# Kernel tuning notes

Measured on AMD Instinct MI355X. Metric: run time of the kernel, lower is better.

Reference implementation:

```python
import jax, jax.numpy as jnp
import numpy as np

# Segmented linear polynomial: irreps '96x0e + 64x1o + 32x2e' -> same
MULS_IN = (96, 64, 32)   # input multiplicities per irrep segment
MULS_OUT = (96, 64, 32)  # output multiplicities per irrep segment
IRREP_DIMS = (1, 3, 5)   # 2l+1 for l = 0, 1, 2
NUM_ELEMENTS = 64        # number of indexed weight sets
BATCH = 16384            # nodes
IN_SIZE = sum(m * d for m, d in zip(MULS_IN, IRREP_DIMS))    # 448
OUT_SIZE = sum(m * d for m, d in zip(MULS_OUT, IRREP_DIMS))  # 448
W_SIZE = sum(mi * mo for mi, mo in zip(MULS_IN, MULS_OUT))   # 14336


def setup_inputs() -> dict:
    key = jax.random.key(0)
    k1, k2, k3 = jax.random.split(key, 3)
    weights = jax.random.normal(k1, (NUM_ELEMENTS, W_SIZE), dtype=jnp.float32)
    x = jax.random.normal(k2, (BATCH, IN_SIZE), dtype=jnp.float32)
    weight_indices = jax.random.randint(k3, (BATCH,), 0, NUM_ELEMENTS, dtype=jnp.int64)
    return {"weights": weights, "x": x, "weight_indices": weight_indices}


def reference(weights, x, weight_indices):
    """Indexed segmented linear: per irrep segment,
    y[b, o, m] = sum_i x[b, i, m] * W[idx[b], i, o]."""
    B = x.shape[0]
    outs = []
    w_off = 0
    x_off = 0
    for mi, mo, d in zip(MULS_IN, MULS_OUT, IRREP_DIMS):
        W_seg = weights[:, w_off:w_off + mi * mo].reshape(-1, mi, mo)  # [E, mi, mo]
        x_seg = x[:, x_off:x_off + mi * d].reshape(B, mi, d)           # [B, mi, d]
        Wg = W_seg[weight_indices]                                     # [B, mi, mo] gather
        y_seg = jnp.einsum('bim,bio->bom', x_seg, Wg)                  # [B, mo, d]
        outs.append(y_seg.reshape(B, mo * d))
        w_off += mi * mo
        x_off += mi * d
    return jnp.concatenate(outs, axis=1)  # [B, OUT_SIZE]
```

## Files before the change

kernel.cpp:

```cpp
#include <hip/hip_runtime.h>


#define BATCH     16384
#define IN_SIZE   448
#define OUT_SIZE  448
#define W_SIZE    14336
#define NELEM     64
#define RTILE     32
#define MAXTILES  576
#define WT_ELEM   15872

typedef __attribute__((ext_vector_type(8))) short short8;
typedef __attribute__((ext_vector_type(8))) unsigned short us8;
typedef __attribute__((ext_vector_type(4))) float f32x4;

__device__ __forceinline__ unsigned short f2bf(float f) {
    unsigned int u = __float_as_uint(f);
    u += 0x7fffu + ((u >> 16) & 1u);
    return (unsigned short)(u >> 16);
}


template <int MI, int MO, int SRC, int DB>
__device__ __forceinline__ void wprep_seg(const float* __restrict__ we,
                                          unsigned short* __restrict__ de,
                                          unsigned short* lw, int t) {
    constexpr int LP  = MO + 4;
    constexpr int STR = MI + 8;
    constexpr int CNT = MI * MO;
    constexpr int C8  = STR / 8;

    for (int g = t * 4; g < CNT; g += 1024) {
        const int i = g / MO, o = g - i * MO;
        const float4 v = *(const float4*)(we + SRC + g);
        ushort4 w = { f2bf(v.x), f2bf(v.y), f2bf(v.z), f2bf(v.w) };
        *(ushort4*)&lw[i * LP + o] = w;
    }
    __syncthreads();

    for (int c = t; c < MO * C8; c += 256) {
        const int o = c / C8, i0 = (c - o * C8) * 8;
        us8 w;
        #pragma unroll
        for (int k = 0; k < 8; ++k)
            w[k] = (i0 + k < MI) ? lw[(i0 + k) * LP + o] : (unsigned short)0;
        *(us8*)&de[DB + o * STR + i0] = w;
    }
}

__global__ __launch_bounds__(256) void combo_kernel(
    const int* __restrict__ widx, const float* __restrict__ weights,
    int* __restrict__ hists, unsigned short* __restrict__ wt) {
    __shared__ __align__(16) unsigned short lw[9600];
    __shared__ int h[NELEM];
    const int t = threadIdx.x;

    if (blockIdx.x < 192) {
        const int e = blockIdx.x / 3, seg = blockIdx.x - 3 * (blockIdx.x / 3);
        const float* __restrict__ we = weights + (size_t)e * W_SIZE;
        unsigned short* __restrict__ de = wt + (size_t)e * WT_ELEM;
        if (seg == 0)      wprep_seg<96, 96,     0,     0>(we, de, lw, t);
        else if (seg == 1) wprep_seg<64, 64,  9216,  9984>(we, de, lw, t);
        else               wprep_seg<32, 32, 13312, 14592>(we, de, lw, t);
        return;
    }
    const int b = blockIdx.x - 192;
    if (t < NELEM) h[t] = 0;
    __syncthreads();
    atomicAdd(&h[widx[b * 256 + t]], 1);
    __syncthreads();
    if (t < NELEM) hists[b * NELEM + t] = h[t];
}


__global__ __launch_bounds__(256) void scatter_kernel(
    const int* __restrict__ widx, const int* __restrict__ hists,
    int* __restrict__ offsets, int* __restrict__ tileoff, int* __restrict__ blk2e,
    int* __restrict__ rowids) {
    __shared__ int tot_s[NELEM], pre_s[NELEM], base_s[NELEM];
    __shared__ int off_s[NELEM + 1], tl_s[NELEM + 1];
    const int b = blockIdx.x, t = threadIdx.x;

    if (t < NELEM) {
        int before = 0, tot = 0;
        for (int c = 0; c < 64; ++c) {
            const int h = hists[c * NELEM + t];
            before += (c < b) ? h : 0;
            tot += h;
        }
        tot_s[t] = tot; pre_s[t] = before;
    }
    __syncthreads();
    if (t == 0) {
        int o = 0, tl = 0;
        for (int e = 0; e < NELEM; ++e) {
            off_s[e] = o; tl_s[e] = tl;
            o += tot_s[e]; tl += (tot_s[e] + RTILE - 1) >> 5;
        }
        off_s[NELEM] = o; tl_s[NELEM] = tl;
    }
    __syncthreads();
    if (t < NELEM) base_s[t] = off_s[t] + pre_s[t];

    if (b == 0) {
        if (t < NELEM) { offsets[t] = off_s[t]; tileoff[t] = tl_s[t]; }
        if (t == 0)    { offsets[NELEM] = off_s[NELEM]; tileoff[NELEM] = tl_s[NELEM]; }
        for (int i = t; i < MAXTILES; i += 256) blk2e[i] = -1;
        __syncthreads();
        if (t < NELEM)
            for (int bb = tl_s[t]; bb < tl_s[t + 1]; ++bb) blk2e[bb] = t;
    }
    __syncthreads();

    const int row = b * 256 + t;
    const int e = widx[row];
    const int pos = atomicAdd(&base_s[e], 1);
    rowids[pos] = row;
}


template <int MI, int MO, int D, int XOFF, int YOFF, int WB>
__device__ __forceinline__ void do_seg(const float* __restrict__ x,
                                       const unsigned short* __restrict__ wt_e,
                                       const int* rid_s, int nrows,
                                       float* __restrict__ out,
                                       unsigned short* lds_w, unsigned short* lds_x,
                                       int t) {
    constexpr int XP   = MI * D + 8;
    constexpr int WSTR = MI + 8;
    constexpr int NT   = MO / 16;
    constexpr int KB   = MI / 32;
    constexpr int MTL  = 2 * D;
    constexpr int WCH  = (MO * WSTR) / 8;
    constexpr int FPT  = (MI * D) / 8;
    constexpr int NQ   = FPT / 4;
    constexpr int MOD  = MO * D;
    constexpr int NTW  = (MTL * NT) / 4;
    constexpr int F4R  = MOD / 4;

    const int r = t >> 3, j = t & 7;

    const float4* __restrict__ src =
        (const float4*)(x + (size_t)rid_s[r] * IN_SIZE + XOFF + j * FPT);
    float vv[FPT];
    #pragma unroll
    for (int q = 0; q < NQ; ++q) {
        const float4 v = src[q];
        vv[q * 4 + 0] = v.x; vv[q * 4 + 1] = v.y;
        vv[q * 4 + 2] = v.z; vv[q * 4 + 3] = v.w;
    }

    const uint4* __restrict__ wsrc = (const uint4*)(wt_e + WB);
    for (int idx = t; idx < WCH; idx += 256) ((uint4*)lds_w)[idx] = wsrc[idx];

    if (D == 1) {
        #pragma unroll
        for (int q = 0; q < NQ; ++q) {
            ushort4 w = { f2bf(vv[q * 4 + 0]), f2bf(vv[q * 4 + 1]),
                          f2bf(vv[q * 4 + 2]), f2bf(vv[q * 4 + 3]) };
            *(ushort4*)&lds_x[r * XP + j * FPT + q * 4] = w;
        }
    } else if (D == 3) {
        #pragma unroll
        for (int m = 0; m < 3; ++m) {
            us8 w;
            #pragma unroll
            for (int bq = 0; bq < 8; ++bq) w[bq] = f2bf(vv[3 * bq + m]);
            *(us8*)&lds_x[r * XP + m * MI + j * 8] = w;
        }
    } else {
        #pragma unroll
        for (int m = 0; m < 5; ++m) {
            ushort4 w = { f2bf(vv[m]), f2bf(vv[5 + m]),
                          f2bf(vv[10 + m]), f2bf(vv[15 + m]) };
            *(ushort4*)&lds_x[r * XP + m * MI + j * 4] = w;
        }
    }
    __syncthreads();

    const int lane = t & 63, w = t >> 6;
    const int row_l = lane & 15, kg = lane >> 4;
    f32x4 accs[NTW];
    #pragma unroll
    for (int q = 0; q < NTW; ++q) {
        const int ct = w + q * 4;
        const int mIdx = ct / NT, nt = ct - mIdx * NT;
        const int mt = mIdx & 1, mch = mIdx >> 1;
        f32x4 acc = {0.f, 0.f, 0.f, 0.f};
        #pragma unroll
        for (int kb = 0; kb < KB; ++kb) {
            const short8 a = *(const short8*)&lds_x[(mt * 16 + row_l) * XP + mch * MI + kb * 32 + kg * 8];
            const short8 b = *(const short8*)&lds_w[(nt * 16 + row_l) * WSTR + kb * 32 + kg * 8];
            acc = __builtin_amdgcn_mfma_f32_16x16x32_bf16(a, b, acc, 0, 0, 0);
        }
        accs[q] = acc;
    }
    __syncthreads();

    float* __restrict__ lout = (float*)lds_w;
    #pragma unroll
    for (int q = 0; q < NTW; ++q) {
        const int ct = w + q * 4;
        const int mIdx = ct / NT, nt = ct - mIdx * NT;
        const int mt = mIdx & 1, mch = mIdx >> 1;
        const int o = nt * 16 + row_l;
        #pragma unroll
        for (int jj = 0; jj < 4; ++jj) {
            const int m = mt * 16 + kg * 4 + jj;
            lout[m * MOD + o * D + mch] = accs[q][jj];
        }
    }
    __syncthreads();

    for (int idx = t; idx < RTILE * F4R; idx += 256) {
        const int rr = idx / F4R, c = idx - rr * F4R;
        if (rr < nrows) {
            float4 v = *(const float4*)&lout[rr * MOD + c * 4];
            *(float4*)&out[(size_t)rid_s[rr] * OUT_SIZE + YOFF + c * 4] = v;
        }
    }
    __syncthreads();
}

__global__ __launch_bounds__(256) void gemm_kernel(
    const float* __restrict__ x, const unsigned short* __restrict__ wt,
    const int* __restrict__ rowids, const int* __restrict__ offsets,
    const int* __restrict__ tileoff, const int* __restrict__ blk2e,
    float* __restrict__ out) {
    __shared__ __align__(16) unsigned short lds[13312];
    __shared__ int rid_s[RTILE];

    const int t   = threadIdx.x;
    const int seg = blockIdx.x / MAXTILES;
    const int tb  = blockIdx.x - seg * MAXTILES;
    const int e   = blk2e[tb];
    if (e < 0) return;
    const int tile  = tb - tileoff[e];
    const int r0    = offsets[e];
    const int cnt   = offsets[e + 1] - r0;
    const int rbase = r0 + tile * RTILE;
    const int nrows = min(RTILE, cnt - tile * RTILE);
    if (t < RTILE) rid_s[t] = rowids[rbase + min(t, nrows - 1)];
    __syncthreads();

    const unsigned short* wt_e = wt + (size_t)e * WT_ELEM;
    if (seg == 0)
        do_seg<96, 96, 1,   0,   0,     0>(x, wt_e, rid_s, nrows, out, lds, lds + 9984, t);
    else if (seg == 1)
        do_seg<64, 64, 3,  96,  96,  9984>(x, wt_e, rid_s, nrows, out, lds, lds + 4608, t);
    else
        do_seg<32, 32, 5, 288, 288, 14592>(x, wt_e, rid_s, nrows, out, lds, lds + 1280, t);
}


extern "C" void kernel_launch(void* const* d_in, const int* in_sizes, int n_in,
                              void* d_out, int out_size, void* d_ws, size_t ws_size,
                              hipStream_t stream) {
    const float* weights = (const float*)d_in[0];
    const float* x       = (const float*)d_in[1];
    const int*   widx    = (const int*)d_in[2];
    float*       out     = (float*)d_out;

    char* ws = (char*)d_ws;
    int* hists   = (int*)(ws + 0);
    int* offsets = (int*)(ws + 16384);
    int* tileoff = (int*)(ws + 16896);
    int* blk2e   = (int*)(ws + 17408);
    int* rowids  = (int*)(ws + 20480);
    unsigned short* wt = (unsigned short*)(ws + 86016);

    combo_kernel  <<<256, 256, 0, stream>>>(widx, weights, hists, wt);
    scatter_kernel<<<64,  256, 0, stream>>>(widx, hists, offsets, tileoff, blk2e, rowids);
    gemm_kernel   <<<3 * MAXTILES, 256, 0, stream>>>(x, wt, rowids, offsets, tileoff, blk2e, out);
}
```

Before: 32.04 us.

## Drop scatter kernel; derive tile row ids in-GEMM via ballot prefix scan

Removes the separate scatter kernel. A single block in the combo kernel now builds the full histogram, offsets and tile map, and each GEMM block rebuilds its own 32 row ids by scanning all weight indices with per-thread bitmasks, a wave prefix sum and popcount. This saves one kernel launch and the rowids buffer round-trip. In exchange every GEMM block reads the whole 64KB index array, and the histogram is done serially by one block. A trailing barrier in the segment routine is also dropped.

```diff
diff --git a/kernel.cpp b/kernel.cpp
--- a/kernel.cpp
+++ b/kernel.cpp
@@ -50,9 +50,9 @@
 
 __global__ __launch_bounds__(256) void combo_kernel(
     const int* __restrict__ widx, const float* __restrict__ weights,
-    int* __restrict__ hists, unsigned short* __restrict__ wt) {
+    int* __restrict__ offsets, int* __restrict__ tileoff, int* __restrict__ blk2e,
+    unsigned short* __restrict__ wt) {
     __shared__ __align__(16) unsigned short lw[9600];
-    __shared__ int h[NELEM];
     const int t = threadIdx.x;
 
     if (blockIdx.x < 192) {
@@ -64,58 +64,28 @@
         else               wprep_seg<32, 32, 13312, 14592>(we, de, lw, t);
         return;
     }
-    const int b = blockIdx.x - 192;
+
+    __shared__ int h[NELEM];
+    __shared__ int off_s[NELEM + 1], tl_s[NELEM + 1];
     if (t < NELEM) h[t] = 0;
     __syncthreads();
-    atomicAdd(&h[widx[b * 256 + t]], 1);
-    __syncthreads();
-    if (t < NELEM) hists[b * NELEM + t] = h[t];
-}
-
-
-__global__ __launch_bounds__(256) void scatter_kernel(
-    const int* __restrict__ widx, const int* __restrict__ hists,
-    int* __restrict__ offsets, int* __restrict__ tileoff, int* __restrict__ blk2e,
-    int* __restrict__ rowids) {
-    __shared__ int tot_s[NELEM], pre_s[NELEM], base_s[NELEM];
-    __shared__ int off_s[NELEM + 1], tl_s[NELEM + 1];
-    const int b = blockIdx.x, t = threadIdx.x;
-
-    if (t < NELEM) {
-        int before = 0, tot = 0;
-        for (int c = 0; c < 64; ++c) {
-            const int h = hists[c * NELEM + t];
-            before += (c < b) ? h : 0;
-            tot += h;
-        }
-        tot_s[t] = tot; pre_s[t] = before;
-    }
+    for (int i = 0; i < 64; ++i)
+        atomicAdd(&h[widx[i * 256 + t]], 1);
     __syncthreads();
     if (t == 0) {
         int o = 0, tl = 0;
         for (int e = 0; e < NELEM; ++e) {
             off_s[e] = o; tl_s[e] = tl;
-            o += tot_s[e]; tl += (tot_s[e] + RTILE - 1) >> 5;
+            o += h[e]; tl += (h[e] + RTILE - 1) >> 5;
         }
         off_s[NELEM] = o; tl_s[NELEM] = tl;
     }
     __syncthreads();
-    if (t < NELEM) base_s[t] = off_s[t] + pre_s[t];
-
-    if (b == 0) {
-        if (t < NELEM) { offsets[t] = off_s[t]; tileoff[t] = tl_s[t]; }
-        if (t == 0)    { offsets[NELEM] = off_s[NELEM]; tileoff[NELEM] = tl_s[NELEM]; }
-        for (int i = t; i < MAXTILES; i += 256) blk2e[i] = -1;
-        __syncthreads();
-        if (t < NELEM)
-            for (int bb = tl_s[t]; bb < tl_s[t + 1]; ++bb) blk2e[bb] = t;
-    }
-    __syncthreads();
-
-    const int row = b * 256 + t;
-    const int e = widx[row];
-    const int pos = atomicAdd(&base_s[e], 1);
-    rowids[pos] = row;
+    if (t <= NELEM) { offsets[t] = off_s[t]; tileoff[t] = tl_s[t]; }
+    for (int i = t; i < MAXTILES; i += 256) blk2e[i] = -1;
+    __syncthreads();
+    if (t < NELEM)
+        for (int bb = tl_s[t]; bb < tl_s[t + 1]; ++bb) blk2e[bb] = t;
 }
 
 
@@ -219,16 +189,16 @@
             *(float4*)&out[(size_t)rid_s[rr] * OUT_SIZE + YOFF + c * 4] = v;
         }
     }
-    __syncthreads();
 }
 
 __global__ __launch_bounds__(256) void gemm_kernel(
     const float* __restrict__ x, const unsigned short* __restrict__ wt,
-    const int* __restrict__ rowids, const int* __restrict__ offsets,
+    const int* __restrict__ widx, const int* __restrict__ offsets,
     const int* __restrict__ tileoff, const int* __restrict__ blk2e,
     float* __restrict__ out) {
     __shared__ __align__(16) unsigned short lds[13312];
     __shared__ int rid_s[RTILE];
+    __shared__ int wsum[4];
 
     const int t   = threadIdx.x;
     const int seg = blockIdx.x / MAXTILES;
@@ -236,12 +206,43 @@
     const int e   = blk2e[tb];
     if (e < 0) return;
     const int tile  = tb - tileoff[e];
-    const int r0    = offsets[e];
-    const int cnt   = offsets[e + 1] - r0;
-    const int rbase = r0 + tile * RTILE;
-    const int nrows = min(RTILE, cnt - tile * RTILE);
-    if (t < RTILE) rid_s[t] = rowids[rbase + min(t, nrows - 1)];
-    __syncthreads();
+    const int cnt   = offsets[e + 1] - offsets[e];
+    const int lo    = tile * RTILE;
+    const int nrows = min(RTILE, cnt - lo);
+
+    {
+        unsigned long long m = 0;
+        #pragma unroll
+        for (int i = 0; i < 64; ++i)
+            m |= (unsigned long long)(widx[i * 256 + t] == e) << i;
+        const int c = __popcll(m);
+        int xacc = c;
+        #pragma unroll
+        for (int d = 1; d < 64; d <<= 1) {
+            const int v = __shfl_up(xacc, d, 64);
+            if ((t & 63) >= d) xacc += v;
+        }
+        if ((t & 63) == 63) wsum[t >> 6] = xacc;
+        __syncthreads();
+        int wbase = 0;
+        #pragma unroll
+        for (int wv = 0; wv < 4; ++wv) wbase += (wv < (t >> 6)) ? wsum[wv] : 0;
+        const int p = wbase + xacc - c;
+        if (p < lo + RTILE && p + c > lo) {
+            unsigned long long mm = m;
+            int k = p;
+            while (mm) {
+                const int i = __ffsll((long long)mm) - 1;
+                if (k >= lo) rid_s[k - lo] = i * 256 + t;
+                ++k;
+                if (k >= lo + RTILE) break;
+                mm &= mm - 1;
+            }
+        }
+        __syncthreads();
+        if (t >= nrows && t < RTILE) rid_s[t] = rid_s[0];
+        __syncthreads();
+    }
 
     const unsigned short* wt_e = wt + (size_t)e * WT_ELEM;
     if (seg == 0)
@@ -262,14 +263,12 @@
     float*       out     = (float*)d_out;
 
     char* ws = (char*)d_ws;
-    int* hists   = (int*)(ws + 0);
-    int* offsets = (int*)(ws + 16384);
-    int* tileoff = (int*)(ws + 16896);
-    int* blk2e   = (int*)(ws + 17408);
-    int* rowids  = (int*)(ws + 20480);
-    unsigned short* wt = (unsigned short*)(ws + 86016);
-
-    combo_kernel  <<<256, 256, 0, stream>>>(widx, weights, hists, wt);
-    scatter_kernel<<<64,  256, 0, stream>>>(widx, hists, offsets, tileoff, blk2e, rowids);
-    gemm_kernel   <<<3 * MAXTILES, 256, 0, stream>>>(x, wt, rowids, offsets, tileoff, blk2e, out);
-}
+    int* offsets = (int*)(ws + 0);
+    int* tileoff = (int*)(ws + 512);
+    int* blk2e   = (int*)(ws + 1024);
+    unsigned short* wt = (unsigned short*)(ws + 8192);
+
+    combo_kernel<<<193, 256, 0, stream>>>(widx, weights, offsets, tileoff, blk2e, wt);
+    gemm_kernel <<<3 * MAXTILES, 256, 0, stream>>>(x, wt, widx, offsets,
+                                                   tileoff, blk2e, out);
+}
```

Result: no change. 31.48 us (-1.7%).
